# Optimization experiments

Hardware: AMD Instinct MI355X
Metric: run time of the kernel (lower is better)

## Reference

```python
import jax, jax.numpy as jnp
import numpy as np

D_MODEL = 1024
N_HEADS = 16
HEAD_DIM = D_MODEL // N_HEADS


def setup_inputs() -> dict:
    key = jax.random.key(0)
    ks = jax.random.split(key, 9)
    s = 0.02
    return {
        "x": jax.random.normal(ks[0], (2, 2048, D_MODEL), jnp.float32),
        "Wk": jax.random.normal(ks[1], (D_MODEL, D_MODEL), jnp.float32) * s,
        "bk": jnp.zeros((D_MODEL,), jnp.float32),
        "Wq": jax.random.normal(ks[2], (D_MODEL, D_MODEL), jnp.float32) * s,
        "bq": jnp.zeros((D_MODEL,), jnp.float32),
        "Wv": jax.random.normal(ks[3], (D_MODEL, D_MODEL), jnp.float32) * s,
        "bv": jnp.zeros((D_MODEL,), jnp.float32),
        "Wp": jax.random.normal(ks[4], (D_MODEL, D_MODEL), jnp.float32) * s,
        "bp": jnp.zeros((D_MODEL,), jnp.float32),
    }


def reference(x, Wk, bk, Wq, bq, Wv, bv, Wp, bp):
    B, T, C = x.shape
    H, Dh = N_HEADS, HEAD_DIM
    # linear projections; torch Linear: y = x @ W.T + b
    def split_heads(y):
        return y.reshape(B, T, H, Dh).transpose(0, 2, 1, 3)  # [B,H,T,Dh]
    k = split_heads(x @ Wk.T + bk)
    q = split_heads(x @ Wq.T + bq)
    v = split_heads(x @ Wv.T + bv)
    scale = 1.0 / jnp.sqrt(jnp.asarray(Dh, x.dtype))
    att = jnp.einsum("bhqd,bhkd->bhqk", q, k) * scale  # [B,H,T,T]
    causal = jnp.tril(jnp.ones((T, T), bool))
    att = jnp.where(causal[None, None], att, -jnp.inf)
    att = jax.nn.softmax(att, axis=-1)
    y = jnp.einsum("bhqk,bhkd->bhqd", att, v)  # [B,H,T,Dh]
    y = y.transpose(0, 2, 1, 3).reshape(B, T, C)
    return y @ Wp.T + bp
```

## Files before the change

kernel.cpp:

```cpp
#include <hip/hip_runtime.h>
#include <stdint.h>

typedef unsigned short u16;
typedef __bf16 bf16x8_t __attribute__((ext_vector_type(8)));
typedef float f32x4 __attribute__((ext_vector_type(4)));

#define T_LEN 2048
#define NHEADS 16
#define DHEAD 64
#define DMODEL 1024
#define QSCALE 0.1803368801111f

__device__ __forceinline__ u16 f2bf(float f) {
  union { float f; uint32_t u; } v; v.f = f;
  uint32_t r = v.u + 0x7FFFu + ((v.u >> 16) & 1u);
  return (u16)(r >> 16);
}

__device__ __forceinline__ void gload16(const u16* g, u16* l) {
  __builtin_amdgcn_global_load_lds((const __attribute__((address_space(1))) void*)g,
                                   (__attribute__((address_space(3))) void*)l, 16, 0, 0);
}

__global__ void cvt_bf16_k(const float* __restrict__ s, u16* __restrict__ d, int n) {
  int i = (blockIdx.x * blockDim.x + threadIdx.x) * 4;
  if (i >= n) return;
  float4 f = *(const float4*)(s + i);
  u16 o[4] = { f2bf(f.x), f2bf(f.y), f2bf(f.z), f2bf(f.w) };
  *(uint2*)(d + i) = *(const uint2*)o;
}

__global__ void cvt_w_k(const float* __restrict__ wq, const float* __restrict__ wk,
                        const float* __restrict__ wv, const float* __restrict__ wp,
                        u16* __restrict__ dqkv, u16* __restrict__ dp) {
  int which = blockIdx.y;
  const float* s = which == 0 ? wq : (which == 1 ? wk : (which == 2 ? wv : wp));
  u16* d = which == 3 ? dp : dqkv + (size_t)which * 1048576;
  int i = (blockIdx.x * blockDim.x + threadIdx.x) * 4;
  float4 f = *(const float4*)(s + i);
  u16 o[4] = { f2bf(f.x), f2bf(f.y), f2bf(f.z), f2bf(f.w) };
  *(uint2*)(d + i) = *(const uint2*)o;
}

template <int TM, int TN, int MODE>
__global__ __launch_bounds__(256, 3) void gemm_k(
    const u16* __restrict__ A, const u16* __restrict__ Bw,
    const float* __restrict__ b0, const float* __restrict__ b1, const float* __restrict__ b2,
    void* __restrict__ o0, void* __restrict__ o1, void* __restrict__ o2,
    int M, int N, int K)
{
  __shared__ __align__(16) u16 As[TM][64];
  __shared__ __align__(16) u16 Bs[TN][64];
  const int m0 = blockIdx.x * TM, n0 = blockIdx.y * TN;
  const int tid = threadIdx.x, lane = tid & 63, w = tid >> 6;
  const int col = lane & 15, quad = lane >> 4;
  constexpr int WM = TM / 2, WN = TN / 2;
  const int wm = (w >> 1) * WM, wn = (w & 1) * WN;
  constexpr int NI = WM / 16, NJ = WN / 16;
  const int rsub = lane >> 3;
  const int csw = ((lane & 7) ^ rsub) * 8;
  const int rx8 = col & 7;

  f32x4 acc[NI][NJ] = {};

  for (int k0 = 0; k0 < K; k0 += 64) {
    __syncthreads();
#pragma unroll
    for (int i = 0; i < TM / 32; i++) {
      int rb = (i * 4 + w) * 8;
      gload16(&A[(size_t)(m0 + rb + rsub) * K + k0 + csw], &As[rb][0]);
    }
#pragma unroll
    for (int i = 0; i < TN / 32; i++) {
      int rb = (i * 4 + w) * 8;
      gload16(&Bw[(size_t)(n0 + rb + rsub) * K + k0 + csw], &Bs[rb][0]);
    }
    __syncthreads();
#pragma unroll
    for (int s = 0; s < 2; s++) {
      bf16x8_t af[NI], bfr[NJ];
#pragma unroll
      for (int i = 0; i < NI; i++) {
        int cp = (quad ^ rx8) ^ (s * 4);
        af[i] = *(const bf16x8_t*)&As[wm + i * 16 + col][cp * 8];
      }
#pragma unroll
      for (int j = 0; j < NJ; j++) {
        int cp = (quad ^ rx8) ^ (s * 4);
        bfr[j] = *(const bf16x8_t*)&Bs[wn + j * 16 + col][cp * 8];
      }
#pragma unroll
      for (int i = 0; i < NI; i++)
#pragma unroll
        for (int j = 0; j < NJ; j++)
          acc[i][j] = __builtin_amdgcn_mfma_f32_16x16x32_bf16(af[i], bfr[j], acc[i][j], 0, 0, 0);
    }
  }

#pragma unroll
  for (int i = 0; i < NI; i++) {
#pragma unroll
    for (int j = 0; j < NJ; j++) {
      int ncol = n0 + wn + j * 16 + col;
      if (MODE == 0) {
        float bias = b0[ncol];
#pragma unroll
        for (int r = 0; r < 4; r++) {
          int m = m0 + wm + i * 16 + quad * 4 + r;
          ((float*)o0)[(size_t)m * N + ncol] = acc[i][j][r] + bias;
        }
      } else {
        int sect = ncol >> 10, nc = ncol & 1023;
        const float* bp = sect == 0 ? b0 : (sect == 1 ? b1 : b2);
        u16* op = sect == 0 ? (u16*)o0 : (sect == 1 ? (u16*)o1 : (u16*)o2);
        float bias = bp[nc];
        float scal = sect == 0 ? QSCALE : 1.0f;
        int h = nc >> 6, d = nc & 63;
#pragma unroll
        for (int r = 0; r < 4; r++) {
          int m = m0 + wm + i * 16 + quad * 4 + r;
          int b = m >> 11, t = m & 2047;
          float v = (acc[i][j][r] + bias) * scal;
          size_t idx = sect < 2 ? ((((size_t)(b * NHEADS + h)) * T_LEN + t) * DHEAD + d)
                                : ((((size_t)(b * NHEADS + h)) * DHEAD + d) * T_LEN + t);
          op[idx] = f2bf(v);
        }
      }
    }
  }
}

__global__ __launch_bounds__(256, 4) void attn_k(
    const u16* __restrict__ Q, const u16* __restrict__ Kb,
    const u16* __restrict__ Vt, u16* __restrict__ Y)
{
  __shared__ __align__(16) u16 Ks[2][64][64];
  __shared__ __align__(16) u16 Vs[2][64][64];
  const int bid = blockIdx.x;
  const int bh = (bid & 7) * 4 + ((bid >> 3) & 3);
  const int qt = 31 - (bid >> 5);
  const int tid = threadIdx.x, lane = tid & 63, w = tid >> 6;
  const int col = lane & 15, quad = lane >> 4;
  const int b = bh >> 4, h = bh & 15;
  const int qw = qt * 64 + w * 16;

  const int rsub = lane >> 3;
  const int csw = ((lane & 7) ^ rsub) * 8;
  const u16* kgb = Kb + (size_t)bh * T_LEN * DHEAD;
  const u16* vgb = Vt + (size_t)bh * DHEAD * T_LEN;
  const int rx = col & 7;

  bf16x8_t qf0, qf1;
  {
    const u16* p = Q + ((size_t)bh * T_LEN + qw + col) * DHEAD + quad * 8;
    qf0 = *(const bf16x8_t*)p;
    qf1 = *(const bf16x8_t*)(p + 32);
  }

  const int qr = qw + col;
  float ls[4] = {0.f, 0.f, 0.f, 0.f};
  f32x4 o[4] = {};

#pragma unroll
  for (int half = 0; half < 2; half++) {
    int rb = w * 16 + half * 8;
    gload16(kgb + (size_t)(rb + rsub) * DHEAD + csw, &Ks[0][rb][0]);
    gload16(vgb + (size_t)(rb + rsub) * T_LEN + csw, &Vs[0][rb][0]);
  }

  for (int kt = 0; kt <= qt; ++kt) {
    const int k0 = kt * 64;
    const int bufi = kt & 1;
    __syncthreads();
    if (kt < qt) {
      const int k0n = k0 + 64, bn = bufi ^ 1;
#pragma unroll
      for (int half = 0; half < 2; half++) {
        int rb = w * 16 + half * 8;
        gload16(kgb + (size_t)(k0n + rb + rsub) * DHEAD + csw, &Ks[bn][rb][0]);
        gload16(vgb + (size_t)(rb + rsub) * T_LEN + k0n + csw, &Vs[bn][rb][0]);
      }
    }

    f32x4 s[4];
#pragma unroll
    for (int nt = 0; nt < 4; nt++) {
      const u16* krow = &Ks[bufi][nt * 16 + col][0];
      bf16x8_t kf0 = *(const bf16x8_t*)(krow + ((quad ^ rx) & 7) * 8);
      bf16x8_t kf1 = *(const bf16x8_t*)(krow + (((4 + quad) ^ rx) & 7) * 8);
      f32x4 a = {};
      a = __builtin_amdgcn_mfma_f32_16x16x32_bf16(kf0, qf0, a, 0, 0, 0);
      a = __builtin_amdgcn_mfma_f32_16x16x32_bf16(kf1, qf1, a, 0, 0, 0);
      s[nt] = a;
    }

    const bool diag = (kt == qt);
    u16 pb[4][4];
#pragma unroll
    for (int nt = 0; nt < 4; nt++) {
#pragma unroll
      for (int r = 0; r < 4; r++) {
        float p = __builtin_amdgcn_exp2f(s[nt][r]);
        if (diag && (k0 + nt * 16 + quad * 4 + r) > qr) p = 0.f;
        uint32_t pu = __float_as_uint(p) & 0xFFFF0000u;
        ls[r] += __uint_as_float(pu);
        pb[nt][r] = (u16)(pu >> 16);
      }
    }
    union PU { bf16x8_t v; u16 h[8]; } pf[2];
#pragma unroll
    for (int r = 0; r < 4; r++) {
      pf[0].h[r] = pb[0][r]; pf[0].h[4 + r] = pb[1][r];
      pf[1].h[r] = pb[2][r]; pf[1].h[4 + r] = pb[3][r];
    }

#pragma unroll
    for (int ks = 0; ks < 2; ks++) {
#pragma unroll
      for (int dt = 0; dt < 4; dt++) {
        const u16* vrow = &Vs[bufi][dt * 16 + col][0];
        union VU { bf16x8_t v; uint2 u2[2]; } va;
        va.u2[0] = *(const uint2*)(vrow + ((ks * 4 + (quad >> 1)) ^ rx) * 8 + (quad & 1) * 4);
        va.u2[1] = *(const uint2*)(vrow + ((ks * 4 + 2 + (quad >> 1)) ^ rx) * 8 + (quad & 1) * 4);
        o[dt] = __builtin_amdgcn_mfma_f32_16x16x32_bf16(va.v, pf[ks].v, o[dt], 0, 0, 0);
      }
    }
  }

  float lsum = (ls[0] + ls[1]) + (ls[2] + ls[3]);
  lsum += __shfl_xor(lsum, 16);
  lsum += __shfl_xor(lsum, 32);
  float inv = 1.0f / lsum;
  int t = qw + col;
#pragma unroll
  for (int dt = 0; dt < 4; dt++) {
    u16 w4[4];
#pragma unroll
    for (int r = 0; r < 4; r++) w4[r] = f2bf(o[dt][r] * inv);
    *(uint2*)&Y[((size_t)(b * T_LEN + t)) * DMODEL + h * DHEAD + dt * 16 + quad * 4] =
        *(const uint2*)w4;
  }
}

extern "C" void kernel_launch(void* const* d_in, const int* in_sizes, int n_in,
                              void* d_out, int out_size, void* d_ws, size_t ws_size,
                              hipStream_t stream) {
  const float* x  = (const float*)d_in[0];
  const float* Wk = (const float*)d_in[1];
  const float* bk = (const float*)d_in[2];
  const float* Wq = (const float*)d_in[3];
  const float* bq = (const float*)d_in[4];
  const float* Wv = (const float*)d_in[5];
  const float* bv = (const float*)d_in[6];
  const float* Wp = (const float*)d_in[7];
  const float* bp = (const float*)d_in[8];

  char* ws = (char*)d_ws;
  const size_t MB = 1u << 20;
  u16* xb    = (u16*)(ws);
  u16* wqkv  = (u16*)(ws + 8 * MB);
  u16* wpb   = (u16*)(ws + 14 * MB);
  u16* qb    = (u16*)(ws + 16 * MB);
  u16* kb    = (u16*)(ws + 24 * MB);
  u16* vtb   = (u16*)(ws + 32 * MB);
  u16* yatt  = (u16*)(ws + 40 * MB);

  cvt_bf16_k<<<4096, 256, 0, stream>>>(x, xb, 4194304);
  dim3 gw(1024, 4);
  cvt_w_k<<<gw, 256, 0, stream>>>(Wq, Wk, Wv, Wp, wqkv, wpb);

  dim3 gqkv(32, 24);
  gemm_k<128, 128, 3><<<gqkv, 256, 0, stream>>>(xb, wqkv, bq, bk, bv,
                                                qb, kb, vtb, 4096, 3072, 1024);

  attn_k<<<1024, 256, 0, stream>>>(qb, kb, vtb, yatt);

  dim3 gp(32, 16);
  gemm_k<128, 64, 0><<<gp, 256, 0, stream>>>(yatt, wpb, bp, nullptr, nullptr,
                                             d_out, nullptr, nullptr, 4096, 1024, 1024);
}
```

Before: 175.8 us.

## Merge conversion kernels, permute V layout, specialise diagonal tile, add MFMA priority

Fuses the x and weight fp32-to-bf16 conversion kernels into a single launch, saving one kernel launch. The QKV GEMM now writes V^T with a permuted token order inside each 64-token block, so the attention kernel can load a V fragment with one 16-byte LDS read instead of two 8-byte reads. The attention loop is split so that only the final diagonal tile carries the causal mask, via a compile-time template flag, and the MFMA sections are wrapped in s_setprio raises. These changes couple the GEMM output layout to the attention read pattern, so any mismatch between the two would give silently wrong results.

```diff
diff --git a/kernel.cpp b/kernel.cpp
--- a/kernel.cpp
+++ b/kernel.cpp
@@ -11,6 +11,8 @@
 #define DMODEL 1024
 #define QSCALE 0.1803368801111f
 
+template <int N> struct IC { static constexpr int v = N; };
+
 __device__ __forceinline__ u16 f2bf(float f) {
   union { float f; uint32_t u; } v; v.f = f;
   uint32_t r = v.u + 0x7FFFu + ((v.u >> 16) & 1u);
@@ -22,21 +24,20 @@
                                    (__attribute__((address_space(3))) void*)l, 16, 0, 0);
 }
 
-__global__ void cvt_bf16_k(const float* __restrict__ s, u16* __restrict__ d, int n) {
-  int i = (blockIdx.x * blockDim.x + threadIdx.x) * 4;
-  if (i >= n) return;
-  float4 f = *(const float4*)(s + i);
-  u16 o[4] = { f2bf(f.x), f2bf(f.y), f2bf(f.z), f2bf(f.w) };
-  *(uint2*)(d + i) = *(const uint2*)o;
-}
-
-__global__ void cvt_w_k(const float* __restrict__ wq, const float* __restrict__ wk,
-                        const float* __restrict__ wv, const float* __restrict__ wp,
-                        u16* __restrict__ dqkv, u16* __restrict__ dp) {
-  int which = blockIdx.y;
-  const float* s = which == 0 ? wq : (which == 1 ? wk : (which == 2 ? wv : wp));
-  u16* d = which == 3 ? dp : dqkv + (size_t)which * 1048576;
-  int i = (blockIdx.x * blockDim.x + threadIdx.x) * 4;
+__global__ void cvt_all_k(const float* __restrict__ x,
+                          const float* __restrict__ wq, const float* __restrict__ wk,
+                          const float* __restrict__ wv, const float* __restrict__ wp,
+                          u16* __restrict__ xb, u16* __restrict__ dqkv, u16* __restrict__ dp) {
+  const float* s; u16* d; int i;
+  if (blockIdx.y == 0) {
+    s = x; d = xb;
+    i = (blockIdx.x * 256 + threadIdx.x) * 4;
+  } else {
+    int which = blockIdx.x >> 10;
+    s = which == 0 ? wq : (which == 1 ? wk : (which == 2 ? wv : wp));
+    d = which == 3 ? dp : dqkv + (size_t)which * 1048576;
+    i = (((blockIdx.x & 1023) * 256) + threadIdx.x) * 4;
+  }
   float4 f = *(const float4*)(s + i);
   u16 o[4] = { f2bf(f.x), f2bf(f.y), f2bf(f.z), f2bf(f.w) };
   *(uint2*)(d + i) = *(const uint2*)o;
@@ -121,8 +122,14 @@
           int m = m0 + wm + i * 16 + quad * 4 + r;
           int b = m >> 11, t = m & 2047;
           float v = (acc[i][j][r] + bias) * scal;
-          size_t idx = sect < 2 ? ((((size_t)(b * NHEADS + h)) * T_LEN + t) * DHEAD + d)
-                                : ((((size_t)(b * NHEADS + h)) * DHEAD + d) * T_LEN + t);
+          size_t idx;
+          if (sect < 2) {
+            idx = (((size_t)(b * NHEADS + h)) * T_LEN + t) * DHEAD + d;
+          } else {
+            int kl = t & 63;
+            int tp = (t & ~63) | (kl & 32) | ((kl & 12) << 1) | ((kl & 16) >> 2) | (kl & 3);
+            idx = (((size_t)(b * NHEADS + h)) * DHEAD + d) * T_LEN + tp;
+          }
           op[idx] = f2bf(v);
         }
       }
@@ -161,28 +168,22 @@
   float ls[4] = {0.f, 0.f, 0.f, 0.f};
   f32x4 o[4] = {};
 
-#pragma unroll
-  for (int half = 0; half < 2; half++) {
-    int rb = w * 16 + half * 8;
-    gload16(kgb + (size_t)(rb + rsub) * DHEAD + csw, &Ks[0][rb][0]);
-    gload16(vgb + (size_t)(rb + rsub) * T_LEN + csw, &Vs[0][rb][0]);
-  }
-
-  for (int kt = 0; kt <= qt; ++kt) {
-    const int k0 = kt * 64;
-    const int bufi = kt & 1;
-    __syncthreads();
-    if (kt < qt) {
-      const int k0n = k0 + 64, bn = bufi ^ 1;
-#pragma unroll
-      for (int half = 0; half < 2; half++) {
-        int rb = w * 16 + half * 8;
-        gload16(kgb + (size_t)(k0n + rb + rsub) * DHEAD + csw, &Ks[bn][rb][0]);
-        gload16(vgb + (size_t)(rb + rsub) * T_LEN + k0n + csw, &Vs[bn][rb][0]);
-      }
-    }
+  auto stage = [&](int ktile) {
+    const int k0n = ktile * 64, bufn = ktile & 1;
+#pragma unroll
+    for (int half = 0; half < 2; half++) {
+      int rb = w * 16 + half * 8;
+      gload16(kgb + (size_t)(k0n + rb + rsub) * DHEAD + csw, &Ks[bufn][rb][0]);
+      gload16(vgb + (size_t)(rb + rsub) * T_LEN + k0n + csw, &Vs[bufn][rb][0]);
+    }
+  };
+
+  auto tile = [&](int kt, auto Mc) {
+    constexpr int M = decltype(Mc)::v;
+    const int k0 = kt * 64, bufi = kt & 1;
 
     f32x4 s[4];
+    __builtin_amdgcn_s_setprio(1);
 #pragma unroll
     for (int nt = 0; nt < 4; nt++) {
       const u16* krow = &Ks[bufi][nt * 16 + col][0];
@@ -193,15 +194,15 @@
       a = __builtin_amdgcn_mfma_f32_16x16x32_bf16(kf1, qf1, a, 0, 0, 0);
       s[nt] = a;
     }
-
-    const bool diag = (kt == qt);
+    __builtin_amdgcn_s_setprio(0);
+
     u16 pb[4][4];
 #pragma unroll
     for (int nt = 0; nt < 4; nt++) {
 #pragma unroll
       for (int r = 0; r < 4; r++) {
         float p = __builtin_amdgcn_exp2f(s[nt][r]);
-        if (diag && (k0 + nt * 16 + quad * 4 + r) > qr) p = 0.f;
+        if (M == 1 && (k0 + nt * 16 + quad * 4 + r) > qr) p = 0.f;
         uint32_t pu = __float_as_uint(p) & 0xFFFF0000u;
         ls[r] += __uint_as_float(pu);
         pb[nt][r] = (u16)(pu >> 16);
@@ -214,18 +215,27 @@
       pf[1].h[r] = pb[2][r]; pf[1].h[4 + r] = pb[3][r];
     }
 
+    __builtin_amdgcn_s_setprio(1);
 #pragma unroll
     for (int ks = 0; ks < 2; ks++) {
 #pragma unroll
       for (int dt = 0; dt < 4; dt++) {
         const u16* vrow = &Vs[bufi][dt * 16 + col][0];
-        union VU { bf16x8_t v; uint2 u2[2]; } va;
-        va.u2[0] = *(const uint2*)(vrow + ((ks * 4 + (quad >> 1)) ^ rx) * 8 + (quad & 1) * 4);
-        va.u2[1] = *(const uint2*)(vrow + ((ks * 4 + 2 + (quad >> 1)) ^ rx) * 8 + (quad & 1) * 4);
-        o[dt] = __builtin_amdgcn_mfma_f32_16x16x32_bf16(va.v, pf[ks].v, o[dt], 0, 0, 0);
-      }
-    }
-  }
+        bf16x8_t va = *(const bf16x8_t*)(vrow + ((ks * 4 + quad) ^ rx) * 8);
+        o[dt] = __builtin_amdgcn_mfma_f32_16x16x32_bf16(va, pf[ks].v, o[dt], 0, 0, 0);
+      }
+    }
+    __builtin_amdgcn_s_setprio(0);
+  };
+
+  stage(0);
+  for (int kt = 0; kt < qt; ++kt) {
+    __syncthreads();
+    stage(kt + 1);
+    tile(kt, IC<0>{});
+  }
+  __syncthreads();
+  tile(qt, IC<1>{});
 
   float lsum = (ls[0] + ls[1]) + (ls[2] + ls[3]);
   lsum += __shfl_xor(lsum, 16);
@@ -265,9 +275,8 @@
   u16* vtb   = (u16*)(ws + 32 * MB);
   u16* yatt  = (u16*)(ws + 40 * MB);
 
-  cvt_bf16_k<<<4096, 256, 0, stream>>>(x, xb, 4194304);
-  dim3 gw(1024, 4);
-  cvt_w_k<<<gw, 256, 0, stream>>>(Wq, Wk, Wv, Wp, wqkv, wpb);
+  dim3 gcv(4096, 2);
+  cvt_all_k<<<gcv, 256, 0, stream>>>(x, Wq, Wk, Wv, Wp, xb, wqkv, wpb);
 
   dim3 gqkv(32, 24);
   gemm_k<128, 128, 3><<<gqkv, 256, 0, stream>>>(xb, wqkv, bq, bk, bv,
```

After: 178.2 us. No clear change (+1.4%).
